# Kernel optimization log

Measured on AMD Instinct MI355X. Metric: run time of the kernel, lower is better.

Reference implementation:

```python
import jax, jax.numpy as jnp
import numpy as np

VX, VY = 0.16, 0.16
X0, Y0 = 0.0, -39.68
BN_EPS = 1e-5
P, M, C_IN, C_OUT = 40000, 100, 9, 64


def setup_inputs() -> dict:
    key = jax.random.key(0)
    ks = jax.random.split(key, 8)
    return {
        "pillar_x": jax.random.normal(ks[0], (P, M), dtype=jnp.float32),
        "pillar_y": jax.random.normal(ks[1], (P, M), dtype=jnp.float32),
        "pillar_z": jax.random.normal(ks[2], (P, M), dtype=jnp.float32),
        "pillar_i": jax.random.uniform(ks[3], (P, M), dtype=jnp.float32),
        "num_points_per_pillar": jax.random.randint(ks[4], (P,), 0, M, dtype=jnp.int32),
        "coors": jax.random.randint(ks[5], (P, 4), 0, 496, dtype=jnp.int32),
        "W": jax.random.normal(ks[6], (C_IN, C_OUT), dtype=jnp.float32) * 0.1,
        "gamma": jnp.ones((C_OUT,), dtype=jnp.float32),
        "beta": jnp.zeros((C_OUT,), dtype=jnp.float32),
    }


def reference(pillar_x, pillar_y, pillar_z, pillar_i, num_points_per_pillar, coors, W, gamma, beta):
    dtype = pillar_x.dtype
    max_points = pillar_x.shape[1]
    # per-pillar point count, clamped to >=1 (matches torch.clamp(min=1))
    n = jnp.clip(num_points_per_pillar, 1, None).astype(dtype)[:, None]  # (P,1)
    mean_x = jnp.sum(pillar_x, axis=1, keepdims=True) / n
    mean_y = jnp.sum(pillar_y, axis=1, keepdims=True) / n
    mean_z = jnp.sum(pillar_z, axis=1, keepdims=True) / n
    x_off = pillar_x - mean_x
    y_off = pillar_y - mean_y
    z_off = pillar_z - mean_z
    # BEV pillar-center coordinates, broadcast over points
    x_bev = (coors[:, 3].astype(dtype) * VX + VX / 2 + X0)[:, None] * jnp.ones((1, max_points), dtype)
    y_bev = (coors[:, 2].astype(dtype) * VY + VY / 2 + Y0)[:, None] * jnp.ones((1, max_points), dtype)
    # validity mask: point index < num_points (vectorized version of the python loop)
    mask = (jnp.arange(max_points)[None, :] < num_points_per_pillar[:, None]).astype(dtype)
    feats = jnp.stack(
        [pillar_x, pillar_y, pillar_z, pillar_i, x_off, y_off, z_off, x_bev, y_bev],
        axis=-1,
    )  # (P, M, 9)
    feats = feats * mask[:, :, None]
    # PFNLayer: Linear (no bias) -> BatchNorm1d (training-mode batch stats) -> ReLU -> max over points
    x = jnp.einsum("pmc,cd->pmd", feats, W)  # (P, M, 64)
    mu = jnp.mean(x, axis=(0, 1))
    var = jnp.var(x, axis=(0, 1))  # biased variance, as BatchNorm uses
    x = (x - mu) * jax.lax.rsqrt(var + BN_EPS) * gamma + beta
    x = jax.nn.relu(x)
    return jnp.max(x, axis=1)  # (P, 64)
```

## Files before the change

### kernel.cpp

```cpp
#include <hip/hip_runtime.h>

#define P_N 40000
#define M_N 100
#define NBF 2500

typedef _Float16 half2_t __attribute__((ext_vector_type(2)));

__device__ __forceinline__ float bcf(int x) { return __int_as_float(x); }
__device__ __forceinline__ int   bci(float x) { return __float_as_int(x); }
__device__ __forceinline__ float rlf(float v, int l) {
  return bcf(__builtin_amdgcn_readlane(bci(v), l));
}
__device__ __forceinline__ int pk16i(float a, float b) {
  return __builtin_bit_cast(int, __builtin_amdgcn_cvt_pkrtz(a, b));
}
__device__ __forceinline__ half2_t h2(int x) { return __builtin_bit_cast(half2_t, x); }
__device__ __forceinline__ int ih2(half2_t v) { return __builtin_bit_cast(int, v); }

__device__ __forceinline__ float dpp_sum64(float x) {
  x += bcf(__builtin_amdgcn_update_dpp(0, bci(x), 0x111, 0xf, 0xf, true));
  x += bcf(__builtin_amdgcn_update_dpp(0, bci(x), 0x112, 0xf, 0xf, true));
  x += bcf(__builtin_amdgcn_update_dpp(0, bci(x), 0x114, 0xf, 0xf, true));
  x += bcf(__builtin_amdgcn_update_dpp(0, bci(x), 0x118, 0xf, 0xf, true));
  x += bcf(__builtin_amdgcn_update_dpp(0, bci(x), 0x142, 0xf, 0xf, true));
  x += bcf(__builtin_amdgcn_update_dpp(0, bci(x), 0x143, 0xf, 0xf, true));
  return x;
}

__device__ __forceinline__ float uPT(int xy, int zi, half2_t AB, half2_t CD, float sE) {
  return __builtin_amdgcn_fdot2(h2(xy), AB,
         __builtin_amdgcn_fdot2(h2(zi), CD, sE, false), false);
}


__global__ __launch_bounds__(256) void k_fused(
    const float* __restrict__ px, const float* __restrict__ py,
    const float* __restrict__ pz, const float* __restrict__ pi,
    const int* __restrict__ npp, const int* __restrict__ coors,
    const float* __restrict__ W,
    float* __restrict__ partials, float* __restrict__ umm)
{
  const int lane = threadIdx.x & 63;
  const int wid  = threadIdx.x >> 6;
  const int d    = lane;

  __shared__ int4  stage[4][64];
  __shared__ float red[4][54];

  float w[9];
  #pragma unroll
  for (int c = 0; c < 9; ++c) w[c] = W[c * 64 + d];
  const float sA = w[0] + w[4], sB = w[1] + w[5], sC = w[2] + w[6], sD = w[3];
  const half2_t AB = h2(pk16i(sA, sB));
  const half2_t CD = h2(pk16i(sC, sD));
  const half2_t H1 = h2(0x3C003C00);

  const bool act = lane < 50;
  const int wgid  = blockIdx.x * 4 + wid;
  const int pbase = __builtin_amdgcn_readfirstlane(wgid * 4);

  const int4 n4 = ((const int4*)npp)[wgid];
  int4 cc[4];
  #pragma unroll
  for (int it = 0; it < 4; ++it) cc[it] = ((const int4*)coors)[pbase + it];

  int u0[4], u1[4], u2[4], u3[4];
  int4 pm[4];
  #pragma unroll
  for (int it = 0; it < 4; ++it) {
    const int p_ = pbase + it;
    float2 X = make_float2(0.f, 0.f), Y = X, Z = X, I = X;
    if (act) {
      X = ((const float2*)(px + (size_t)p_ * M_N))[lane];
      Y = ((const float2*)(py + (size_t)p_ * M_N))[lane];
      Z = ((const float2*)(pz + (size_t)p_ * M_N))[lane];
      I = ((const float2*)(pi + (size_t)p_ * M_N))[lane];
    }
    u0[it] = pk16i(X.x, X.y);
    u1[it] = pk16i(Y.x, Y.y);
    u2[it] = pk16i(Z.x, Z.y);
    u3[it] = pk16i(I.x, I.y);
    pm[it].x = pk16i(X.x, Y.x);
    pm[it].y = pk16i(Z.x, I.x);
    pm[it].z = pk16i(X.y, Y.y);
    pm[it].w = pk16i(Z.y, I.y);
  }

  float a1[9] = {};
  float a2[45] = {};

  #pragma unroll
  for (int it = 0; it < 4; ++it) {
    const int p_ = pbase + it;
    const int n  = ((const int*)&n4)[it];

    float sx = __builtin_amdgcn_fdot2(h2(u0[it]), H1, 0.f, false);
    float sy = __builtin_amdgcn_fdot2(h2(u1[it]), H1, 0.f, false);
    float sz = __builtin_amdgcn_fdot2(h2(u2[it]), H1, 0.f, false);
    sx = dpp_sum64(sx); sy = dpp_sum64(sy); sz = dpp_sum64(sz);
    const int nc = n < 1 ? 1 : n;
    const float inv = __builtin_amdgcn_rcpf((float)nc);
    const float mx = rlf(sx, 63) * inv;
    const float my = rlf(sy, 63) * inv;
    const float mz = rlf(sz, 63) * inv;

    const float xb = fmaf((float)cc[it].w, 0.16f, 0.08f);
    const float yb = fmaf((float)cc[it].z, 0.16f, 0.08f - 39.68f);

    const unsigned m0 = (2 * lane     < n) ? 0x0000FFFFu : 0u;
    const unsigned m1 = (2 * lane + 1 < n) ? 0xFFFF0000u : 0u;
    const unsigned msk = m0 | m1;

    const half2_t MX = h2(pk16i(mx, mx));
    const half2_t MY = h2(pk16i(my, my));
    const half2_t MZ = h2(pk16i(mz, mz));

    int g[9];
    g[0] = u0[it] & msk;
    g[1] = u1[it] & msk;
    g[2] = u2[it] & msk;
    g[3] = u3[it] & msk;
    g[4] = ih2(h2(u0[it]) - MX) & msk;
    g[5] = ih2(h2(u1[it]) - MY) & msk;
    g[6] = ih2(h2(u2[it]) - MZ) & msk;
    g[7] = pk16i(xb, xb) & msk;
    g[8] = pk16i(yb, yb) & msk;

    #pragma unroll
    for (int c = 0; c < 9; ++c)
      a1[c] = __builtin_amdgcn_fdot2(h2(g[c]), H1, a1[c], false);
    {
      int k = 0;
      #pragma unroll
      for (int c = 0; c < 9; ++c) {
        #pragma unroll
        for (int c2 = c; c2 < 9; ++c2) {
          a2[k] = __builtin_amdgcn_fdot2(h2(g[c]), h2(g[c2]), a2[k], false);
          ++k;
        }
      }
    }

    const float sE = fmaf(-mx, w[4], fmaf(-my, w[5], fmaf(-mz, w[6],
                     fmaf(xb, w[7], yb * w[8]))));

    stage[wid][lane] = pm[it];
    const int4* sp = &stage[wid][0];

    float um0 = -3.0e38f, um1 = -3.0e38f;
    const int nq = n >> 2;
    for (int l = 0; l < nq; ++l) {
      const int4 qa = sp[2 * l];
      const int4 qb = sp[2 * l + 1];
      const float v0 = uPT(qa.x, qa.y, AB, CD, sE);
      const float v1 = uPT(qa.z, qa.w, AB, CD, sE);
      const float v2 = uPT(qb.x, qb.y, AB, CD, sE);
      const float v3 = uPT(qb.z, qb.w, AB, CD, sE);
      um0 = fmaxf(fmaxf(um0, v0), v1);
      um1 = fmaxf(fmaxf(um1, v2), v3);
    }
    const int m_ = nq * 4;
    if (n - m_ >= 2) {
      const int4 qa = sp[m_ >> 1];
      const float v0 = uPT(qa.x, qa.y, AB, CD, sE);
      const float v1 = uPT(qa.z, qa.w, AB, CD, sE);
      um0 = fmaxf(fmaxf(um0, v0), v1);
    }
    if (n & 1) {
      const int2 qq = ((const int2*)sp)[n - 1];
      um1 = fmaxf(um1, uPT(qq.x, qq.y, AB, CD, sE));
    }
    umm[(size_t)p_ * 64 + d] = fmaxf(um0, um1);
  }

  #pragma unroll
  for (int i = 0; i < 9; ++i)  a1[i] = dpp_sum64(a1[i]);
  #pragma unroll
  for (int i = 0; i < 45; ++i) a2[i] = dpp_sum64(a2[i]);

  if (lane == 63) {
    #pragma unroll
    for (int i = 0; i < 9; ++i)  red[wid][i]     = a1[i];
    #pragma unroll
    for (int i = 0; i < 45; ++i) red[wid][9 + i] = a2[i];
  }
  __syncthreads();
  if (threadIdx.x < 54) {
    const int t = threadIdx.x;
    partials[blockIdx.x * 54 + t] = red[0][t] + red[1][t] + red[2][t] + red[3][t];
  }
}


__global__ __launch_bounds__(256) void k_red(
    const float* __restrict__ partials, float* __restrict__ moments)
{
  const int c = blockIdx.x;
  float s = 0.f;
  for (int b = threadIdx.x; b < NBF; b += 256) s += partials[b * 54 + c];
  s = dpp_sum64(s);
  __shared__ float r4[4];
  const int lane = threadIdx.x & 63, wid = threadIdx.x >> 6;
  if (lane == 63) r4[wid] = s;
  __syncthreads();
  if (threadIdx.x == 0) moments[c] = r4[0] + r4[1] + r4[2] + r4[3];
}


__global__ __launch_bounds__(64) void k_stats(
    const float* __restrict__ moments, const float* __restrict__ W,
    const float* __restrict__ gamma, const float* __restrict__ beta,
    float* __restrict__ scale, float* __restrict__ shift)
{
  const int d = threadIdx.x;
  float mom[54];
  #pragma unroll
  for (int i = 0; i < 54; ++i) mom[i] = moments[i];

  float w[9];
  #pragma unroll
  for (int c = 0; c < 9; ++c) w[c] = W[c * 64 + d];
  const float invN = 1.f / ((float)P_N * (float)M_N);
  float mu = 0.f;
  #pragma unroll
  for (int c = 0; c < 9; ++c) mu += mom[c] * w[c];
  mu *= invN;
  float e2 = 0.f;
  int k = 0;
  #pragma unroll
  for (int c = 0; c < 9; ++c) {
    #pragma unroll
    for (int c2 = c; c2 < 9; ++c2) {
      const float t = w[c] * w[c2] * mom[9 + k];
      e2 += (c == c2) ? t : 2.f * t;
      ++k;
    }
  }
  e2 *= invN;
  float var = e2 - mu * mu;
  var = var < 0.f ? 0.f : var;
  const float sc = gamma[d] * rsqrtf(var + 1e-5f);
  const float sh = fmaf(-mu, sc, beta[d]);
  scale[d] = sc;
  shift[d] = sh;
}


__global__ __launch_bounds__(256) void k_apply(
    const int* __restrict__ npp, const float* __restrict__ scale,
    const float* __restrict__ shift, float* __restrict__ out)
{
  const int gid = blockIdx.x * 256 + threadIdx.x;
  const int p = gid >> 4;
  const int q = gid & 15;

  float4 u4 = ((const float4*)out)[gid];
  const float4 sc4 = ((const float4*)scale)[q];
  const float4 sh4 = ((const float4*)shift)[q];
  const int n = npp[p];
  const bool has_masked = n < M_N;

  float4 r;
  float t;
  t = fmaf(sc4.x, u4.x, sh4.x); if (has_masked) t = fmaxf(t, sh4.x); r.x = fmaxf(t, 0.f);
  t = fmaf(sc4.y, u4.y, sh4.y); if (has_masked) t = fmaxf(t, sh4.y); r.y = fmaxf(t, 0.f);
  t = fmaf(sc4.z, u4.z, sh4.z); if (has_masked) t = fmaxf(t, sh4.z); r.z = fmaxf(t, 0.f);
  t = fmaf(sc4.w, u4.w, sh4.w); if (has_masked) t = fmaxf(t, sh4.w); r.w = fmaxf(t, 0.f);
  ((float4*)out)[gid] = r;
}


extern "C" void kernel_launch(void* const* d_in, const int* in_sizes, int n_in,
                              void* d_out, int out_size, void* d_ws, size_t ws_size,
                              hipStream_t stream) {
  const float* px    = (const float*)d_in[0];
  const float* py    = (const float*)d_in[1];
  const float* pz    = (const float*)d_in[2];
  const float* pi    = (const float*)d_in[3];
  const int*   npp   = (const int*)d_in[4];
  const int*   coors = (const int*)d_in[5];
  const float* W     = (const float*)d_in[6];
  const float* gamma = (const float*)d_in[7];
  const float* beta  = (const float*)d_in[8];
  float* out = (float*)d_out;

  float* wsf      = (float*)d_ws;
  float* partials = wsf;
  float* moments  = wsf + 135000;
  float* scale    = wsf + 135072;
  float* shift    = wsf + 135136;

  k_fused<<<NBF, 256, 0, stream>>>(px, py, pz, pi, npp, coors, W, partials, out);
  k_red<<<54, 256, 0, stream>>>(partials, moments);
  k_stats<<<1, 64, 0, stream>>>(moments, W, gamma, beta, scale, shift);
  k_apply<<<P_N * 64 / 4 / 256, 256, 0, stream>>>(npp, scale, shift, out);
}
```

Before: 56.54 us.

## Stage all four pillars in LDS up front and software-pipeline the point-max loop

Each pillar's packed points now go into its own LDS slot at load time, so the staging no longer has to be redone and read back inside the per-pillar loop. The means, BEV centres, and moment accumulation are split into separate loops over the four pillars ahead of the max loop. That loop now prefetches the next pair of LDS quads while the current pair is being computed, and the tail is handled with a single rem-based branch. The aim is to hide LDS and reduction latency through more independent work, at the cost of four times the LDS and more live registers, and the prefetch reads two quads past the last needed index.

Result: no change. 57.65 us (+2.0%).

```diff
diff --git a/kernel.cpp b/kernel.cpp
--- a/kernel.cpp
+++ b/kernel.cpp
@@ -44,7 +44,7 @@
   const int wid  = threadIdx.x >> 6;
   const int d    = lane;
 
-  __shared__ int4  stage[4][64];
+  __shared__ int4  stage[4][4][64];
   __shared__ float red[4][54];
 
   float w[9];
@@ -65,7 +65,6 @@
   for (int it = 0; it < 4; ++it) cc[it] = ((const int4*)coors)[pbase + it];
 
   int u0[4], u1[4], u2[4], u3[4];
-  int4 pm[4];
   #pragma unroll
   for (int it = 0; it < 4; ++it) {
     const int p_ = pbase + it;
@@ -80,41 +79,45 @@
     u1[it] = pk16i(Y.x, Y.y);
     u2[it] = pk16i(Z.x, Z.y);
     u3[it] = pk16i(I.x, I.y);
-    pm[it].x = pk16i(X.x, Y.x);
-    pm[it].y = pk16i(Z.x, I.x);
-    pm[it].z = pk16i(X.y, Y.y);
-    pm[it].w = pk16i(Z.y, I.y);
+    int4 pm;
+    pm.x = pk16i(X.x, Y.x);
+    pm.y = pk16i(Z.x, I.x);
+    pm.z = pk16i(X.y, Y.y);
+    pm.w = pk16i(Z.y, I.y);
+    stage[wid][it][lane] = pm;
+  }
+
+  float sx[4], sy[4], sz[4];
+  #pragma unroll
+  for (int it = 0; it < 4; ++it) {
+    sx[it] = dpp_sum64(__builtin_amdgcn_fdot2(h2(u0[it]), H1, 0.f, false));
+    sy[it] = dpp_sum64(__builtin_amdgcn_fdot2(h2(u1[it]), H1, 0.f, false));
+    sz[it] = dpp_sum64(__builtin_amdgcn_fdot2(h2(u2[it]), H1, 0.f, false));
+  }
+  float mxv[4], myv[4], mzv[4], xbv[4], ybv[4];
+  #pragma unroll
+  for (int it = 0; it < 4; ++it) {
+    const int n  = ((const int*)&n4)[it];
+    const int nc = n < 1 ? 1 : n;
+    const float inv = __builtin_amdgcn_rcpf((float)nc);
+    mxv[it] = rlf(sx[it], 63) * inv;
+    myv[it] = rlf(sy[it], 63) * inv;
+    mzv[it] = rlf(sz[it], 63) * inv;
+    xbv[it] = fmaf((float)cc[it].w, 0.16f, 0.08f);
+    ybv[it] = fmaf((float)cc[it].z, 0.16f, 0.08f - 39.68f);
   }
 
   float a1[9] = {};
   float a2[45] = {};
-
-  #pragma unroll
-  for (int it = 0; it < 4; ++it) {
-    const int p_ = pbase + it;
-    const int n  = ((const int*)&n4)[it];
-
-    float sx = __builtin_amdgcn_fdot2(h2(u0[it]), H1, 0.f, false);
-    float sy = __builtin_amdgcn_fdot2(h2(u1[it]), H1, 0.f, false);
-    float sz = __builtin_amdgcn_fdot2(h2(u2[it]), H1, 0.f, false);
-    sx = dpp_sum64(sx); sy = dpp_sum64(sy); sz = dpp_sum64(sz);
-    const int nc = n < 1 ? 1 : n;
-    const float inv = __builtin_amdgcn_rcpf((float)nc);
-    const float mx = rlf(sx, 63) * inv;
-    const float my = rlf(sy, 63) * inv;
-    const float mz = rlf(sz, 63) * inv;
-
-    const float xb = fmaf((float)cc[it].w, 0.16f, 0.08f);
-    const float yb = fmaf((float)cc[it].z, 0.16f, 0.08f - 39.68f);
-
+  #pragma unroll
+  for (int it = 0; it < 4; ++it) {
+    const int n = ((const int*)&n4)[it];
     const unsigned m0 = (2 * lane     < n) ? 0x0000FFFFu : 0u;
     const unsigned m1 = (2 * lane + 1 < n) ? 0xFFFF0000u : 0u;
     const unsigned msk = m0 | m1;
-
-    const half2_t MX = h2(pk16i(mx, mx));
-    const half2_t MY = h2(pk16i(my, my));
-    const half2_t MZ = h2(pk16i(mz, mz));
-
+    const half2_t MX = h2(pk16i(mxv[it], mxv[it]));
+    const half2_t MY = h2(pk16i(myv[it], myv[it]));
+    const half2_t MZ = h2(pk16i(mzv[it], mzv[it]));
     int g[9];
     g[0] = u0[it] & msk;
     g[1] = u1[it] & msk;
@@ -123,53 +126,48 @@
     g[4] = ih2(h2(u0[it]) - MX) & msk;
     g[5] = ih2(h2(u1[it]) - MY) & msk;
     g[6] = ih2(h2(u2[it]) - MZ) & msk;
-    g[7] = pk16i(xb, xb) & msk;
-    g[8] = pk16i(yb, yb) & msk;
-
+    g[7] = pk16i(xbv[it], xbv[it]) & msk;
+    g[8] = pk16i(ybv[it], ybv[it]) & msk;
     #pragma unroll
     for (int c = 0; c < 9; ++c)
       a1[c] = __builtin_amdgcn_fdot2(h2(g[c]), H1, a1[c], false);
-    {
-      int k = 0;
+    int k = 0;
+    #pragma unroll
+    for (int c = 0; c < 9; ++c) {
       #pragma unroll
-      for (int c = 0; c < 9; ++c) {
-        #pragma unroll
-        for (int c2 = c; c2 < 9; ++c2) {
-          a2[k] = __builtin_amdgcn_fdot2(h2(g[c]), h2(g[c2]), a2[k], false);
-          ++k;
-        }
+      for (int c2 = c; c2 < 9; ++c2) {
+        a2[k] = __builtin_amdgcn_fdot2(h2(g[c]), h2(g[c2]), a2[k], false);
+        ++k;
       }
     }
-
-    const float sE = fmaf(-mx, w[4], fmaf(-my, w[5], fmaf(-mz, w[6],
-                     fmaf(xb, w[7], yb * w[8]))));
-
-    stage[wid][lane] = pm[it];
-    const int4* sp = &stage[wid][0];
+  }
+
+  #pragma unroll
+  for (int it = 0; it < 4; ++it) {
+    const int p_ = pbase + it;
+    const int n  = ((const int*)&n4)[it];
+    const float sE = fmaf(-mxv[it], w[4], fmaf(-myv[it], w[5], fmaf(-mzv[it], w[6],
+                     fmaf(xbv[it], w[7], ybv[it] * w[8]))));
+    const int4* sp = &stage[wid][it][0];
 
     float um0 = -3.0e38f, um1 = -3.0e38f;
-    const int nq = n >> 2;
+    const int nq  = n >> 2;
+    const int rem = n & 3;
+    int4 qa = sp[0], qb = sp[1];
     for (int l = 0; l < nq; ++l) {
-      const int4 qa = sp[2 * l];
-      const int4 qb = sp[2 * l + 1];
+      const int4 pa = sp[2 * l + 2];
+      const int4 pb = sp[2 * l + 3];
       const float v0 = uPT(qa.x, qa.y, AB, CD, sE);
       const float v1 = uPT(qa.z, qa.w, AB, CD, sE);
       const float v2 = uPT(qb.x, qb.y, AB, CD, sE);
       const float v3 = uPT(qb.z, qb.w, AB, CD, sE);
       um0 = fmaxf(fmaxf(um0, v0), v1);
       um1 = fmaxf(fmaxf(um1, v2), v3);
-    }
-    const int m_ = nq * 4;
-    if (n - m_ >= 2) {
-      const int4 qa = sp[m_ >> 1];
-      const float v0 = uPT(qa.x, qa.y, AB, CD, sE);
-      const float v1 = uPT(qa.z, qa.w, AB, CD, sE);
-      um0 = fmaxf(fmaxf(um0, v0), v1);
-    }
-    if (n & 1) {
-      const int2 qq = ((const int2*)sp)[n - 1];
-      um1 = fmaxf(um1, uPT(qq.x, qq.y, AB, CD, sE));
-    }
+      qa = pa; qb = pb;
+    }
+    if (rem >= 1) um0 = fmaxf(um0, uPT(qa.x, qa.y, AB, CD, sE));
+    if (rem >= 2) um0 = fmaxf(um0, uPT(qa.z, qa.w, AB, CD, sE));
+    if (rem >= 3) um1 = fmaxf(um1, uPT(qb.x, qb.y, AB, CD, sE));
     umm[(size_t)p_ * 64 + d] = fmaxf(um0, um1);
   }
 
```

## Compute BN second moments analytically from per-pillar sums instead of per-point products

Applied to the files above, without the earlier changes.

Replaces the 54 per-point fdot2 moment accumulations and their 54 wave reductions with 10 raw-feature cross products plus per-pillar scalar sums. Each lane computes one moment's correction term in closed form using the pillar means and BEV centres. k_stats then reassembles the full moment matrix. Staging of points into LDS is also split per pillar so the writes happen up front. The cost is more branchy per-lane selection logic and a slightly different numerical path, since offsets are no longer rounded to fp16 per point.

After: 55.58 us. Within noise of the previous version (-1.7%).

```diff
diff --git a/kernel.cpp b/kernel.cpp
--- a/kernel.cpp
+++ b/kernel.cpp
@@ -3,6 +3,8 @@
 #define P_N 40000
 #define M_N 100
 #define NBF 2500
+#define NPART 80
+#define NUSED 74
 
 typedef _Float16 half2_t __attribute__((ext_vector_type(2)));
 
@@ -15,7 +17,9 @@
   return __builtin_bit_cast(int, __builtin_amdgcn_cvt_pkrtz(a, b));
 }
 __device__ __forceinline__ half2_t h2(int x) { return __builtin_bit_cast(half2_t, x); }
-__device__ __forceinline__ int ih2(half2_t v) { return __builtin_bit_cast(int, v); }
+__device__ __forceinline__ float dot2(int a, int b, float acc) {
+  return __builtin_amdgcn_fdot2(h2(a), h2(b), acc, false);
+}
 
 __device__ __forceinline__ float dpp_sum64(float x) {
   x += bcf(__builtin_amdgcn_update_dpp(0, bci(x), 0x111, 0xf, 0xf, true));
@@ -44,16 +48,29 @@
   const int wid  = threadIdx.x >> 6;
   const int d    = lane;
 
-  __shared__ int4  stage[4][64];
-  __shared__ float red[4][54];
+  __shared__ int4  stage[4][4][64];
+  __shared__ float red[4][NPART];
+
+  int c = 9, c2 = 9;
+  if (lane < 45) {
+    int k = lane; c = 0;
+    while (k >= 9 - c) { k -= 9 - c; ++c; }
+    c2 = c + k;
+  } else if (lane < 54) {
+    c = lane - 45; c2 = 9;
+  }
+  const int rc1 = (c  < 4) ? c  : (c  < 7) ? c  - 4 : (c  < 9) ? c  - 2 : 4;
+  const int rc2 = (c2 < 4) ? c2 : (c2 < 7) ? c2 - 4 : (c2 < 9) ? c2 - 2 : 4;
+  const bool bothVec = (rc1 < 4) && (rc2 < 4);
+  const bool statln  = lane < 54;
 
   float w[9];
   #pragma unroll
-  for (int c = 0; c < 9; ++c) w[c] = W[c * 64 + d];
+  for (int q = 0; q < 9; ++q) w[q] = W[q * 64 + d];
   const float sA = w[0] + w[4], sB = w[1] + w[5], sC = w[2] + w[6], sD = w[3];
   const half2_t AB = h2(pk16i(sA, sB));
   const half2_t CD = h2(pk16i(sC, sD));
-  const half2_t H1 = h2(0x3C003C00);
+  const int H1 = 0x3C003C00;
 
   const bool act = lane < 50;
   const int wgid  = blockIdx.x * 4 + wid;
@@ -65,7 +82,6 @@
   for (int it = 0; it < 4; ++it) cc[it] = ((const int4*)coors)[pbase + it];
 
   int u0[4], u1[4], u2[4], u3[4];
-  int4 pm[4];
   #pragma unroll
   for (int it = 0; it < 4; ++it) {
     const int p_ = pbase + it;
@@ -80,73 +96,84 @@
     u1[it] = pk16i(Y.x, Y.y);
     u2[it] = pk16i(Z.x, Z.y);
     u3[it] = pk16i(I.x, I.y);
-    pm[it].x = pk16i(X.x, Y.x);
-    pm[it].y = pk16i(Z.x, I.x);
-    pm[it].z = pk16i(X.y, Y.y);
-    pm[it].w = pk16i(Z.y, I.y);
-  }
-
-  float a1[9] = {};
-  float a2[45] = {};
+    int4 pm;
+    pm.x = pk16i(X.x, Y.x);
+    pm.y = pk16i(Z.x, I.x);
+    pm.z = pk16i(X.y, Y.y);
+    pm.w = pk16i(Z.y, I.y);
+    stage[wid][it][lane] = pm;
+  }
+
+  float R2a[10] = {};
+  float corrAcc = 0.f;
 
   #pragma unroll
   for (int it = 0; it < 4; ++it) {
     const int p_ = pbase + it;
     const int n  = ((const int*)&n4)[it];
-
-    float sx = __builtin_amdgcn_fdot2(h2(u0[it]), H1, 0.f, false);
-    float sy = __builtin_amdgcn_fdot2(h2(u1[it]), H1, 0.f, false);
-    float sz = __builtin_amdgcn_fdot2(h2(u2[it]), H1, 0.f, false);
-    sx = dpp_sum64(sx); sy = dpp_sum64(sy); sz = dpp_sum64(sz);
+    const float nf = (float)n;
+
+    const unsigned msk = ((2 * lane     < n) ? 0x0000FFFFu : 0u)
+                       | ((2 * lane + 1 < n) ? 0xFFFF0000u : 0u);
+    const int g0 = u0[it] & msk;
+    const int g1 = u1[it] & msk;
+    const int g2 = u2[it] & msk;
+    const int g3 = u3[it] & msk;
+
+    float fx = dot2(u0[it], H1, 0.f);
+    float fy = dot2(u1[it], H1, 0.f);
+    float fz = dot2(u2[it], H1, 0.f);
+    float vx = dot2(g0, H1, 0.f);
+    float vy = dot2(g1, H1, 0.f);
+    float vz = dot2(g2, H1, 0.f);
+    float vi = dot2(g3, H1, 0.f);
+    fx = dpp_sum64(fx); fy = dpp_sum64(fy); fz = dpp_sum64(fz);
+    vx = dpp_sum64(vx); vy = dpp_sum64(vy); vz = dpp_sum64(vz); vi = dpp_sum64(vi);
+
     const int nc = n < 1 ? 1 : n;
     const float inv = __builtin_amdgcn_rcpf((float)nc);
-    const float mx = rlf(sx, 63) * inv;
-    const float my = rlf(sy, 63) * inv;
-    const float mz = rlf(sz, 63) * inv;
+    const float mx = rlf(fx, 63) * inv;
+    const float my = rlf(fy, 63) * inv;
+    const float mz = rlf(fz, 63) * inv;
+    const float svx = rlf(vx, 63);
+    const float svy = rlf(vy, 63);
+    const float svz = rlf(vz, 63);
+    const float svi = rlf(vi, 63);
 
     const float xb = fmaf((float)cc[it].w, 0.16f, 0.08f);
     const float yb = fmaf((float)cc[it].z, 0.16f, 0.08f - 39.68f);
 
-    const unsigned m0 = (2 * lane     < n) ? 0x0000FFFFu : 0u;
-    const unsigned m1 = (2 * lane + 1 < n) ? 0xFFFF0000u : 0u;
-    const unsigned msk = m0 | m1;
-
-    const half2_t MX = h2(pk16i(mx, mx));
-    const half2_t MY = h2(pk16i(my, my));
-    const half2_t MZ = h2(pk16i(mz, mz));
-
-    int g[9];
-    g[0] = u0[it] & msk;
-    g[1] = u1[it] & msk;
-    g[2] = u2[it] & msk;
-    g[3] = u3[it] & msk;
-    g[4] = ih2(h2(u0[it]) - MX) & msk;
-    g[5] = ih2(h2(u1[it]) - MY) & msk;
-    g[6] = ih2(h2(u2[it]) - MZ) & msk;
-    g[7] = pk16i(xb, xb) & msk;
-    g[8] = pk16i(yb, yb) & msk;
-
-    #pragma unroll
-    for (int c = 0; c < 9; ++c)
-      a1[c] = __builtin_amdgcn_fdot2(h2(g[c]), H1, a1[c], false);
+    R2a[0] = dot2(g0, g0, R2a[0]);
+    R2a[1] = dot2(g0, g1, R2a[1]);
+    R2a[2] = dot2(g0, g2, R2a[2]);
+    R2a[3] = dot2(g0, g3, R2a[3]);
+    R2a[4] = dot2(g1, g1, R2a[4]);
+    R2a[5] = dot2(g1, g2, R2a[5]);
+    R2a[6] = dot2(g1, g3, R2a[6]);
+    R2a[7] = dot2(g2, g2, R2a[7]);
+    R2a[8] = dot2(g2, g3, R2a[8]);
+    R2a[9] = dot2(g3, g3, R2a[9]);
+
     {
-      int k = 0;
-      #pragma unroll
-      for (int c = 0; c < 9; ++c) {
-        #pragma unroll
-        for (int c2 = c; c2 < 9; ++c2) {
-          a2[k] = __builtin_amdgcn_fdot2(h2(g[c]), h2(g[c2]), a2[k], false);
-          ++k;
-        }
-      }
+      const float nxb = nf * xb, nyb = nf * yb;
+      const float S1 = (rc1 == 0) ? svx : (rc1 == 1) ? svy : (rc1 == 2) ? svz
+                     : (rc1 == 3) ? svi : (rc1 == 4) ? nf  : (rc1 == 5) ? nxb : nyb;
+      const float S2 = (rc2 == 0) ? svx : (rc2 == 1) ? svy : (rc2 == 2) ? svz
+                     : (rc2 == 3) ? svi : (rc2 == 4) ? nf  : (rc2 == 5) ? nxb : nyb;
+      float base = 0.f;
+      if (!bothVec)
+        base = (rc1 > 3) ? ((rc1 == 4) ? S2 : (rc1 == 5) ? xb * S2 : yb * S2)
+                         : ((rc2 == 4) ? S1 : (rc2 == 5) ? xb * S1 : yb * S1);
+      const float mv1 = (c  == 4) ? mx : (c  == 5) ? my : (c  == 6) ? mz : 0.f;
+      const float mv2 = (c2 == 4) ? mx : (c2 == 5) ? my : (c2 == 6) ? mz : 0.f;
+      const float term = base - mv1 * S2 - mv2 * S1 + nf * mv1 * mv2;
+      if (statln) corrAcc += term;
     }
 
     const float sE = fmaf(-mx, w[4], fmaf(-my, w[5], fmaf(-mz, w[6],
                      fmaf(xb, w[7], yb * w[8]))));
 
-    stage[wid][lane] = pm[it];
-    const int4* sp = &stage[wid][0];
-
+    const int4* sp = &stage[wid][it][0];
     float um0 = -3.0e38f, um1 = -3.0e38f;
     const int nq = n >> 2;
     for (int l = 0; l < nq; ++l) {
@@ -174,65 +201,88 @@
   }
 
   #pragma unroll
-  for (int i = 0; i < 9; ++i)  a1[i] = dpp_sum64(a1[i]);
-  #pragma unroll
-  for (int i = 0; i < 45; ++i) a2[i] = dpp_sum64(a2[i]);
-
+  for (int i = 0; i < 10; ++i) R2a[i] = dpp_sum64(R2a[i]);
+
+  red[wid][lane] = corrAcc;
   if (lane == 63) {
     #pragma unroll
-    for (int i = 0; i < 9; ++i)  red[wid][i]     = a1[i];
-    #pragma unroll
-    for (int i = 0; i < 45; ++i) red[wid][9 + i] = a2[i];
+    for (int i = 0; i < 10; ++i) red[wid][64 + i] = R2a[i];
   }
   __syncthreads();
-  if (threadIdx.x < 54) {
+  if (threadIdx.x < NUSED) {
     const int t = threadIdx.x;
-    partials[blockIdx.x * 54 + t] = red[0][t] + red[1][t] + red[2][t] + red[3][t];
+    partials[blockIdx.x * NPART + t] = red[0][t] + red[1][t] + red[2][t] + red[3][t];
   }
 }
 
 
 __global__ __launch_bounds__(256) void k_red(
-    const float* __restrict__ partials, float* __restrict__ moments)
+    const float* __restrict__ partials, float* __restrict__ stats)
 {
   const int c = blockIdx.x;
   float s = 0.f;
-  for (int b = threadIdx.x; b < NBF; b += 256) s += partials[b * 54 + c];
+  for (int b = threadIdx.x; b < NBF; b += 256) s += partials[b * NPART + c];
   s = dpp_sum64(s);
   __shared__ float r4[4];
   const int lane = threadIdx.x & 63, wid = threadIdx.x >> 6;
   if (lane == 63) r4[wid] = s;
   __syncthreads();
-  if (threadIdx.x == 0) moments[c] = r4[0] + r4[1] + r4[2] + r4[3];
+  if (threadIdx.x == 0) stats[c] = r4[0] + r4[1] + r4[2] + r4[3];
 }
 
 
 __global__ __launch_bounds__(64) void k_stats(
-    const float* __restrict__ moments, const float* __restrict__ W,
+    const float* __restrict__ stats, const float* __restrict__ W,
     const float* __restrict__ gamma, const float* __restrict__ beta,
     float* __restrict__ scale, float* __restrict__ shift)
 {
   const int d = threadIdx.x;
-  float mom[54];
-  #pragma unroll
-  for (int i = 0; i < 54; ++i) mom[i] = moments[i];
+  __shared__ float Cs[NUSED];
+  Cs[d] = stats[d];
+  if (d < NUSED - 64) Cs[64 + d] = stats[64 + d];
+  __syncthreads();
+
+  float mom1[9];
+  #pragma unroll
+  for (int q = 0; q < 9; ++q) mom1[q] = Cs[45 + q];
+  float mom2[45];
+  {
+    int k = 0;
+    #pragma unroll
+    for (int cA = 0; cA < 9; ++cA) {
+      #pragma unroll
+      for (int cB = cA; cB < 9; ++cB) {
+        float v = Cs[k];
+        if (cA <= 6 && cB <= 6) {
+          const int a = (cA < 4) ? cA : cA - 4;
+          const int b = (cB < 4) ? cB : cB - 4;
+          const int lo = a < b ? a : b;
+          const int hi = a < b ? b : a;
+          const int idx = lo * 4 - lo * (lo - 1) / 2 + (hi - lo);
+          v += Cs[64 + idx];
+        }
+        mom2[k] = v;
+        ++k;
+      }
+    }
+  }
 
   float w[9];
   #pragma unroll
-  for (int c = 0; c < 9; ++c) w[c] = W[c * 64 + d];
+  for (int q = 0; q < 9; ++q) w[q] = W[q * 64 + d];
   const float invN = 1.f / ((float)P_N * (float)M_N);
   float mu = 0.f;
   #pragma unroll
-  for (int c = 0; c < 9; ++c) mu += mom[c] * w[c];
+  for (int q = 0; q < 9; ++q) mu += mom1[q] * w[q];
   mu *= invN;
   float e2 = 0.f;
   int k = 0;
   #pragma unroll
-  for (int c = 0; c < 9; ++c) {
+  for (int cA = 0; cA < 9; ++cA) {
     #pragma unroll
-    for (int c2 = c; c2 < 9; ++c2) {
-      const float t = w[c] * w[c2] * mom[9 + k];
-      e2 += (c == c2) ? t : 2.f * t;
+    for (int cB = cA; cB < 9; ++cB) {
+      const float t = w[cA] * w[cB] * mom2[k];
+      e2 += (cA == cB) ? t : 2.f * t;
       ++k;
     }
   }
@@ -286,12 +336,12 @@
 
   float* wsf      = (float*)d_ws;
   float* partials = wsf;
-  float* moments  = wsf + 135000;
-  float* scale    = wsf + 135072;
-  float* shift    = wsf + 135136;
+  float* stats    = wsf + 200000;
+  float* scale    = wsf + 200128;
+  float* shift    = wsf + 200192;
 
   k_fused<<<NBF, 256, 0, stream>>>(px, py, pz, pi, npp, coors, W, partials, out);
-  k_red<<<54, 256, 0, stream>>>(partials, moments);
-  k_stats<<<1, 64, 0, stream>>>(moments, W, gamma, beta, scale, shift);
+  k_red<<<NUSED, 256, 0, stream>>>(partials, stats);
+  k_stats<<<1, 64, 0, stream>>>(stats, W, gamma, beta, scale, shift);
   k_apply<<<P_N * 64 / 4 / 256, 256, 0, stream>>>(npp, scale, shift, out);
 }
```
